# Kernel optimization log

Hardware: AMD Instinct MI355X
Metric: run time of the kernel (lower is better)

Reference implementation:

```python
import jax, jax.numpy as jnp
import numpy as np

B = 4096
D = 1024
WEIGHT = 1.0
EPS = 1e-7  # Keras K.epsilon()


def setup_inputs() -> dict:
    key = jax.random.key(0)
    k1, k2 = jax.random.split(key)
    return {
        "left": jax.random.normal(k1, (B, D), dtype=jnp.float32),
        "right": jax.random.normal(k2, (B, D), dtype=jnp.float32),
        "temperature": jnp.zeros((1,), dtype=jnp.float32),
    }


def _l2_normalize(x):
    # matches l2_norm: sqrt(max(sum(x^2), eps))
    sq = jnp.sum(jnp.square(x), axis=-1, keepdims=True)
    return x / jnp.sqrt(jnp.maximum(sq, EPS))


def reference(left, right, temperature):
    ln = _l2_normalize(left)   # [B, D]
    rn = _l2_normalize(right)  # [B, D]
    scale = jnp.exp(temperature)  # (1,) broadcasts
    logits_left = jnp.einsum("bd,cd->bc", ln, rn) * scale   # [B, B]
    logits_right = logits_left.T                             # rn @ ln.T * scale
    prob_left = jax.nn.softmax(logits_left, axis=-1)
    prob_right = jax.nn.softmax(logits_right, axis=-1)
    # NOTE: the original calls CCE(prob, labels), i.e. y_true=prob, y_pred=eye.
    # Keras clips y_pred to [eps, 1-eps]; loss = -sum(y_true * log(clip(y_pred))).
    labels = jnp.eye(B, dtype=jnp.float32)
    log_clipped = jnp.log(jnp.clip(labels, EPS, 1.0 - EPS))  # diag: log(1-eps), off: log(eps)
    loss_left = -jnp.sum(prob_left * log_clipped)
    loss_right = -jnp.sum(prob_right * log_clipped)
    loss = (loss_left + loss_right) / 2.0 / B
    return WEIGHT * loss
```

## Files before the change

kernel.cpp:

```cpp
#include <hip/hip_runtime.h>
#include <hip/hip_bf16.h>

#define Bn 4096
#define Dk 1024
#define EPSF 1e-7f

typedef float f32x4 __attribute__((ext_vector_type(4)));
typedef long long2_t __attribute__((ext_vector_type(2)));

__device__ __forceinline__ void async_copy16(const void* g, void* l) {
    __builtin_amdgcn_global_load_lds((__attribute__((address_space(1))) void*)(uintptr_t)g,
                                     (__attribute__((address_space(3))) void*)l, 16, 0, 0);
}

__global__ __launch_bounds__(256)
void nrm_kernel(const float4* __restrict__ left, const float4* __restrict__ right,
                unsigned char* __restrict__ lnb8, unsigned char* __restrict__ rnb8,
                float* __restrict__ diag, float* __restrict__ rowsum,
                float* __restrict__ colsum)
{
    const int row = blockIdx.x;
    const int t = threadIdx.x;
    const int idx = row * (Dk / 4) + t;
    const float4 l = left[idx];
    const float4 r = right[idx];
    float sl = l.x * l.x + l.y * l.y + l.z * l.z + l.w * l.w;
    float sr = r.x * r.x + r.y * r.y + r.z * r.z + r.w * r.w;
    float slr = l.x * r.x + l.y * r.y + l.z * r.z + l.w * r.w;
    #pragma unroll
    for (int off = 1; off < 64; off <<= 1) {
        sl += __shfl_xor(sl, off);
        sr += __shfl_xor(sr, off);
        slr += __shfl_xor(slr, off);
    }
    __shared__ float red[3][4];
    const int wave = t >> 6, lane = t & 63;
    if (lane == 0) { red[0][wave] = sl; red[1][wave] = sr; red[2][wave] = slr; }
    __syncthreads();
    sl = red[0][0] + red[0][1] + red[0][2] + red[0][3];
    sr = red[1][0] + red[1][1] + red[1][2] + red[1][3];
    const float invl = 1.0f / sqrtf(fmaxf(sl, EPSF));
    const float invr = 1.0f / sqrtf(fmaxf(sr, EPSF));
    const float sL = 8.0f * invl;
    const float sR = 8.0f * invr;
    int pkL = __builtin_amdgcn_cvt_pk_fp8_f32(l.x * sL, l.y * sL, 0, false);
    pkL = __builtin_amdgcn_cvt_pk_fp8_f32(l.z * sL, l.w * sL, pkL, true);
    int pkR = __builtin_amdgcn_cvt_pk_fp8_f32(r.x * sR, r.y * sR, 0, false);
    pkR = __builtin_amdgcn_cvt_pk_fp8_f32(r.z * sR, r.w * sR, pkR, true);
    const int k0 = 4 * t;
    const int g = k0 >> 6;
    const int kl = k0 & 63;
    const int dst = row * Dk + (g << 6) + (((kl & 31) >> 3) << 4) + ((kl >> 5) << 3) + (kl & 7);
    *(unsigned*)(lnb8 + dst) = (unsigned)pkL;
    *(unsigned*)(rnb8 + dst) = (unsigned)pkR;
    if (t == 0) {
        const float d = red[2][0] + red[2][1] + red[2][2] + red[2][3];
        diag[row] = d * invl * invr;
        rowsum[row] = 0.f;
        colsum[row] = 0.f;
    }
}

__global__ __launch_bounds__(256, 2)
void gemm_sm_kernel(const unsigned char* __restrict__ lnb8,
                    const unsigned char* __restrict__ rnb8,
                    const float* __restrict__ temp,
                    float* __restrict__ rowsum, float* __restrict__ colsum)
{
    __shared__ __align__(16) unsigned char As[2][128 * 64];
    __shared__ __align__(16) unsigned char Bs[2][256 * 64];

    const int tid = threadIdx.x;
    const int wave = tid >> 6;
    const int lane = tid & 63;
    const int bm0 = blockIdx.y * 128;
    const int bn0 = blockIdx.x * 256;

    const int srow = lane >> 2;
    const int sj = lane & 3;
    int goffA[2], lofsA[2];
    #pragma unroll
    for (int i = 0; i < 2; ++i) {
        const int rloc = wave * 32 + i * 16 + srow;
        goffA[i] = rloc * Dk + 16 * (sj ^ ((rloc >> 1) & 3));
        lofsA[i] = (wave * 32 + i * 16) * 64;
    }
    int goffB[4], lofsB[4];
    #pragma unroll
    for (int i = 0; i < 4; ++i) {
        const int rloc = wave * 64 + i * 16 + srow;
        goffB[i] = rloc * Dk + 16 * (sj ^ ((rloc >> 1) & 3));
        lofsB[i] = (wave * 64 + i * 16) * 64;
    }
    const unsigned char* baseA = lnb8 + (size_t)bm0 * Dk;
    const unsigned char* baseB = rnb8 + (size_t)bn0 * Dk;

    const int wm = (wave & 1) * 64;
    const int wn = (wave >> 1) * 128;
    const int quad = lane >> 4;
    const int r16 = lane & 15;
    const int skey = (r16 >> 1) & 3;
    const int gq = 16 * (quad ^ skey);
    int aoff[4], boff[8];
    #pragma unroll
    for (int i = 0; i < 4; ++i)
        aoff[i] = (wm + i * 16 + r16) * 64 + gq;
    #pragma unroll
    for (int i = 0; i < 8; ++i)
        boff[i] = (wn + i * 16 + r16) * 64 + gq;

    f32x4 acc[4][8];
    #pragma unroll
    for (int i = 0; i < 4; ++i)
        #pragma unroll
        for (int j = 0; j < 8; ++j)
            acc[i][j] = (f32x4){0.f, 0.f, 0.f, 0.f};

    #pragma unroll
    for (int i = 0; i < 2; ++i) async_copy16(baseA + goffA[i], &As[0][lofsA[i]]);
    #pragma unroll
    for (int i = 0; i < 4; ++i) async_copy16(baseB + goffB[i], &Bs[0][lofsB[i]]);

    #pragma unroll 2
    for (int it = 0; it < 16; ++it) {
        const int cur = it & 1;
        const int nxt = cur ^ 1;
        const int knext = ((it + 1) & 15) * 64;
        #pragma unroll
        for (int i = 0; i < 2; ++i) async_copy16(baseA + goffA[i] + knext, &As[nxt][lofsA[i]]);
        #pragma unroll
        for (int i = 0; i < 4; ++i) async_copy16(baseB + goffB[i] + knext, &Bs[nxt][lofsB[i]]);
        asm volatile("s_waitcnt vmcnt(6)\n\ts_barrier" ::: "memory");
        long2_t af01[4], bf01[8];
        #pragma unroll
        for (int i = 0; i < 4; ++i) af01[i] = *(const long2_t*)(&As[cur][aoff[i]]);
        #pragma unroll
        for (int i = 0; i < 8; ++i) bf01[i] = *(const long2_t*)(&Bs[cur][boff[i]]);
        #pragma unroll
        for (int mi = 0; mi < 4; ++mi)
            #pragma unroll
            for (int ni = 0; ni < 8; ++ni)
                acc[mi][ni] = __builtin_amdgcn_mfma_f32_16x16x32_fp8_fp8(
                    af01[mi].x, bf01[ni].x, acc[mi][ni], 0, 0, 0);
        #pragma unroll
        for (int mi = 0; mi < 4; ++mi)
            #pragma unroll
            for (int ni = 0; ni < 8; ++ni)
                acc[mi][ni] = __builtin_amdgcn_mfma_f32_16x16x32_fp8_fp8(
                    af01[mi].y, bf01[ni].y, acc[mi][ni], 0, 0, 0);
        asm volatile("s_barrier" ::: "memory");
    }

    const float scale = __expf(temp[0]);
    const float dq = 0.015625f * scale;
    #pragma unroll
    for (int mi = 0; mi < 4; ++mi)
        #pragma unroll
        for (int ni = 0; ni < 8; ++ni)
            #pragma unroll
            for (int r = 0; r < 4; ++r)
                acc[mi][ni][r] = __expf(dq * acc[mi][ni][r] - scale);

    #pragma unroll
    for (int mi = 0; mi < 4; ++mi) {
        #pragma unroll
        for (int r = 0; r < 4; ++r) {
            float v = 0.f;
            #pragma unroll
            for (int ni = 0; ni < 8; ++ni) v += acc[mi][ni][r];
            v += __shfl_xor(v, 1);
            v += __shfl_xor(v, 2);
            v += __shfl_xor(v, 4);
            v += __shfl_xor(v, 8);
            if (r16 == 0)
                atomicAdd(&rowsum[bm0 + wm + mi * 16 + quad * 4 + r], v);
        }
    }
    #pragma unroll
    for (int ni = 0; ni < 8; ++ni) {
        float v = 0.f;
        #pragma unroll
        for (int mi = 0; mi < 4; ++mi)
            #pragma unroll
            for (int r = 0; r < 4; ++r)
                v += acc[mi][ni][r];
        v += __shfl_xor(v, 16);
        v += __shfl_xor(v, 32);
        if (quad == 0)
            atomicAdd(&colsum[bn0 + wn + ni * 16 + r16], v);
    }
}

__global__ __launch_bounds__(256)
void loss_kernel(const float* __restrict__ diag, const float* __restrict__ rowsum,
                 const float* __restrict__ colsum, const float* __restrict__ temp,
                 float* __restrict__ out)
{
    const int t = threadIdx.x;
    const float scale = __expf(temp[0]);
    float dL = 0.f, dR = 0.f;
    for (int i = t; i < Bn; i += 256) {
        const float e = __expf(scale * (diag[i] - 1.0f));
        dL += e * __builtin_amdgcn_rcpf(rowsum[i]);
        dR += e * __builtin_amdgcn_rcpf(colsum[i]);
    }
    #pragma unroll
    for (int off = 1; off < 64; off <<= 1) {
        dL += __shfl_xor(dL, off);
        dR += __shfl_xor(dR, off);
    }
    __shared__ float rd[2][4];
    const int wave = t >> 6, lane = t & 63;
    if (lane == 0) { rd[0][wave] = dL; rd[1][wave] = dR; }
    __syncthreads();
    if (t == 0) {
        dL = rd[0][0] + rd[0][1] + rd[0][2] + rd[0][3];
        dR = rd[1][0] + rd[1][1] + rd[1][2] + rd[1][3];
        const float logeps = logf(EPSF);
        const float log1m = logf(1.0f - EPSF);
        const float lossL = -(dL * log1m + ((float)Bn - dL) * logeps);
        const float lossR = -(dR * log1m + ((float)Bn - dR) * logeps);
        out[0] = (lossL + lossR) * 0.5f / (float)Bn;
    }
}

extern "C" void kernel_launch(void* const* d_in, const int* in_sizes, int n_in,
                              void* d_out, int out_size, void* d_ws, size_t ws_size,
                              hipStream_t stream) {
    (void)in_sizes; (void)n_in; (void)out_size; (void)ws_size;
    const float* left = (const float*)d_in[0];
    const float* right = (const float*)d_in[1];
    const float* temp = (const float*)d_in[2];

    char* ws = (char*)d_ws;
    unsigned char* lnb8 = (unsigned char*)ws;
    unsigned char* rnb8 = (unsigned char*)(ws + (size_t)Bn * Dk);
    float* diag = (float*)(ws + 2 * (size_t)Bn * Dk);
    float* rowsum = diag + Bn;
    float* colsum = rowsum + Bn;

    nrm_kernel<<<Bn, 256, 0, stream>>>((const float4*)left, (const float4*)right,
                                       lnb8, rnb8, diag, rowsum, colsum);
    dim3 g2(Bn / 256, Bn / 128);
    gemm_sm_kernel<<<g2, 256, 0, stream>>>(lnb8, rnb8, temp, rowsum, colsum);
    loss_kernel<<<1, 256, 0, stream>>>(diag, rowsum, colsum, temp, (float*)d_out);
}
```

Baseline: 114.2 us.

## Switch GEMM to 32x32x64 scaled FP8 MFMA with simplified operand layout

Replaces the 16x16x32 FP8 MFMA tiling (4x8 tiles, two k-halves) with the gfx950 mfma_scale 32x32x64 f8f6f4 instruction on 2x4 tiles of 32x32, using unit scales. The normalize kernel now writes FP8 rows in natural order, and the LDS read offsets are rebuilt so each lane gathers 32 contiguous K bytes from two swizzled 16-byte chunks. The goal is fewer, larger MFMA issues per K step and fewer LDS reads. The row and column reductions are rewritten for the 32x32 accumulator layout, which brings more shuffle steps and carries a risk of layout mistakes.

```diff
diff --git a/kernel.cpp b/kernel.cpp
--- a/kernel.cpp
+++ b/kernel.cpp
@@ -5,8 +5,9 @@
 #define Dk 1024
 #define EPSF 1e-7f
 
-typedef float f32x4 __attribute__((ext_vector_type(4)));
-typedef long long2_t __attribute__((ext_vector_type(2)));
+typedef float f32x16 __attribute__((ext_vector_type(16)));
+typedef int i32x4 __attribute__((ext_vector_type(4)));
+typedef int i32x8 __attribute__((ext_vector_type(8)));
 
 __device__ __forceinline__ void async_copy16(const void* g, void* l) {
     __builtin_amdgcn_global_load_lds((__attribute__((address_space(1))) void*)(uintptr_t)g,
@@ -47,10 +48,7 @@
     pkL = __builtin_amdgcn_cvt_pk_fp8_f32(l.z * sL, l.w * sL, pkL, true);
     int pkR = __builtin_amdgcn_cvt_pk_fp8_f32(r.x * sR, r.y * sR, 0, false);
     pkR = __builtin_amdgcn_cvt_pk_fp8_f32(r.z * sR, r.w * sR, pkR, true);
-    const int k0 = 4 * t;
-    const int g = k0 >> 6;
-    const int kl = k0 & 63;
-    const int dst = row * Dk + (g << 6) + (((kl & 31) >> 3) << 4) + ((kl >> 5) << 3) + (kl & 7);
+    const int dst = row * Dk + 4 * t;
     *(unsigned*)(lnb8 + dst) = (unsigned)pkL;
     *(unsigned*)(rnb8 + dst) = (unsigned)pkR;
     if (t == 0) {
@@ -97,24 +95,32 @@
 
     const int wm = (wave & 1) * 64;
     const int wn = (wave >> 1) * 128;
-    const int quad = lane >> 4;
-    const int r16 = lane & 15;
-    const int skey = (r16 >> 1) & 3;
-    const int gq = 16 * (quad ^ skey);
-    int aoff[4], boff[8];
-    #pragma unroll
-    for (int i = 0; i < 4; ++i)
-        aoff[i] = (wm + i * 16 + r16) * 64 + gq;
-    #pragma unroll
-    for (int i = 0; i < 8; ++i)
-        boff[i] = (wn + i * 16 + r16) * 64 + gq;
-
-    f32x4 acc[4][8];
-    #pragma unroll
-    for (int i = 0; i < 4; ++i)
-        #pragma unroll
-        for (int j = 0; j < 8; ++j)
-            acc[i][j] = (f32x4){0.f, 0.f, 0.f, 0.f};
+    const int r32 = lane & 31;
+    const int h = lane >> 5;
+    int aoff[2][2], boff[4][2];
+    #pragma unroll
+    for (int mi = 0; mi < 2; ++mi) {
+        const int row = wm + mi * 32 + r32;
+        const int key = (row >> 1) & 3;
+        aoff[mi][0] = row * 64 + 16 * ((2 * h) ^ key);
+        aoff[mi][1] = row * 64 + 16 * ((2 * h + 1) ^ key);
+    }
+    #pragma unroll
+    for (int ni = 0; ni < 4; ++ni) {
+        const int row = wn + ni * 32 + r32;
+        const int key = (row >> 1) & 3;
+        boff[ni][0] = row * 64 + 16 * ((2 * h) ^ key);
+        boff[ni][1] = row * 64 + 16 * ((2 * h + 1) ^ key);
+    }
+
+    f32x16 acc[2][4];
+    #pragma unroll
+    for (int mi = 0; mi < 2; ++mi)
+        #pragma unroll
+        for (int ni = 0; ni < 4; ++ni)
+            #pragma unroll
+            for (int r = 0; r < 16; ++r)
+                acc[mi][ni][r] = 0.f;
 
     #pragma unroll
     for (int i = 0; i < 2; ++i) async_copy16(baseA + goffA[i], &As[0][lofsA[i]]);
@@ -131,63 +137,66 @@
         #pragma unroll
         for (int i = 0; i < 4; ++i) async_copy16(baseB + goffB[i] + knext, &Bs[nxt][lofsB[i]]);
         asm volatile("s_waitcnt vmcnt(6)\n\ts_barrier" ::: "memory");
-        long2_t af01[4], bf01[8];
-        #pragma unroll
-        for (int i = 0; i < 4; ++i) af01[i] = *(const long2_t*)(&As[cur][aoff[i]]);
-        #pragma unroll
-        for (int i = 0; i < 8; ++i) bf01[i] = *(const long2_t*)(&Bs[cur][boff[i]]);
-        #pragma unroll
-        for (int mi = 0; mi < 4; ++mi)
-            #pragma unroll
-            for (int ni = 0; ni < 8; ++ni)
-                acc[mi][ni] = __builtin_amdgcn_mfma_f32_16x16x32_fp8_fp8(
-                    af01[mi].x, bf01[ni].x, acc[mi][ni], 0, 0, 0);
-        #pragma unroll
-        for (int mi = 0; mi < 4; ++mi)
-            #pragma unroll
-            for (int ni = 0; ni < 8; ++ni)
-                acc[mi][ni] = __builtin_amdgcn_mfma_f32_16x16x32_fp8_fp8(
-                    af01[mi].y, bf01[ni].y, acc[mi][ni], 0, 0, 0);
+        i32x8 af[2], bf[4];
+        #pragma unroll
+        for (int mi = 0; mi < 2; ++mi) {
+            const i32x4 lo = *(const i32x4*)(&As[cur][aoff[mi][0]]);
+            const i32x4 hi = *(const i32x4*)(&As[cur][aoff[mi][1]]);
+            af[mi] = __builtin_shufflevector(lo, hi, 0, 1, 2, 3, 4, 5, 6, 7);
+        }
+        #pragma unroll
+        for (int ni = 0; ni < 4; ++ni) {
+            const i32x4 lo = *(const i32x4*)(&Bs[cur][boff[ni][0]]);
+            const i32x4 hi = *(const i32x4*)(&Bs[cur][boff[ni][1]]);
+            bf[ni] = __builtin_shufflevector(lo, hi, 0, 1, 2, 3, 4, 5, 6, 7);
+        }
+        #pragma unroll
+        for (int mi = 0; mi < 2; ++mi)
+            #pragma unroll
+            for (int ni = 0; ni < 4; ++ni)
+                acc[mi][ni] = __builtin_amdgcn_mfma_scale_f32_32x32x64_f8f6f4(
+                    af[mi], bf[ni], acc[mi][ni],
+                    0, 0,
+                    0, 0x7f7f7f7f,
+                    0, 0x7f7f7f7f);
         asm volatile("s_barrier" ::: "memory");
     }
 
     const float scale = __expf(temp[0]);
     const float dq = 0.015625f * scale;
     #pragma unroll
-    for (int mi = 0; mi < 4; ++mi)
-        #pragma unroll
-        for (int ni = 0; ni < 8; ++ni)
-            #pragma unroll
-            for (int r = 0; r < 4; ++r)
+    for (int mi = 0; mi < 2; ++mi)
+        #pragma unroll
+        for (int ni = 0; ni < 4; ++ni)
+            #pragma unroll
+            for (int r = 0; r < 16; ++r)
                 acc[mi][ni][r] = __expf(dq * acc[mi][ni][r] - scale);
 
     #pragma unroll
-    for (int mi = 0; mi < 4; ++mi) {
-        #pragma unroll
-        for (int r = 0; r < 4; ++r) {
-            float v = 0.f;
-            #pragma unroll
-            for (int ni = 0; ni < 8; ++ni) v += acc[mi][ni][r];
+    for (int mi = 0; mi < 2; ++mi) {
+        #pragma unroll
+        for (int r = 0; r < 16; ++r) {
+            float v = acc[mi][0][r] + acc[mi][1][r] + acc[mi][2][r] + acc[mi][3][r];
             v += __shfl_xor(v, 1);
             v += __shfl_xor(v, 2);
             v += __shfl_xor(v, 4);
             v += __shfl_xor(v, 8);
-            if (r16 == 0)
-                atomicAdd(&rowsum[bm0 + wm + mi * 16 + quad * 4 + r], v);
+            v += __shfl_xor(v, 16);
+            if (r32 == 0)
+                atomicAdd(&rowsum[bm0 + wm + mi * 32 + (r & 3) + 8 * (r >> 2) + 4 * h], v);
         }
     }
     #pragma unroll
-    for (int ni = 0; ni < 8; ++ni) {
+    for (int ni = 0; ni < 4; ++ni) {
         float v = 0.f;
         #pragma unroll
-        for (int mi = 0; mi < 4; ++mi)
-            #pragma unroll
-            for (int r = 0; r < 4; ++r)
+        for (int mi = 0; mi < 2; ++mi)
+            #pragma unroll
+            for (int r = 0; r < 16; ++r)
                 v += acc[mi][ni][r];
-        v += __shfl_xor(v, 16);
         v += __shfl_xor(v, 32);
-        if (quad == 0)
-            atomicAdd(&colsum[bn0 + wn + ni * 16 + r16], v);
+        if (h == 0)
+            atomicAdd(&colsum[bn0 + wn + ni * 32 + r32], v);
     }
 }
 
```

Result: faster. 106.8 us (-6.5%).
